# Kernel tuning notes

Measured on AMD Instinct MI355X. Metric: run time of the kernel, lower is better.

## Reference

```python
import jax, jax.numpy as jnp
import numpy as np

N = 100000      # nodes
E = 3200000     # edges (avg degree 32)
DIN, DH, DOUT = 256, 256, 64
K = 10          # propagation hops


def _uniform(key, shape, fan_in):
    b = 1.0 / np.sqrt(fan_in)
    return jax.random.uniform(key, shape, jnp.float32, -b, b)


def setup_inputs() -> dict:
    key = jax.random.key(0)
    ks = jax.random.split(key, 8)
    x = jax.random.normal(ks[0], (N, DIN), jnp.float32)
    edge_index = jax.random.randint(ks[1], (2, E), 0, N, dtype=jnp.int64)
    W1 = _uniform(ks[2], (DIN, DH), DIN)
    b1 = _uniform(ks[3], (DH,), DIN)
    W2 = _uniform(ks[4], (DH, DOUT), DH)
    b2 = _uniform(ks[5], (DOUT,), DH)
    proj_w = _uniform(ks[6], (DOUT,), DOUT)
    proj_b = _uniform(ks[7], (), DOUT)
    return {"x": x, "edge_index": edge_index, "W1": W1, "b1": b1,
            "W2": W2, "b2": b2, "proj_w": proj_w, "proj_b": proj_b}


def _gcn_norm(edge_index, num_nodes):
    # add self-loops with weight 1, symmetric normalization deg^-1/2 A deg^-1/2
    loops = jnp.arange(num_nodes, dtype=edge_index.dtype)
    row = jnp.concatenate([edge_index[0], loops])
    col = jnp.concatenate([edge_index[1], loops])
    w = jnp.ones(row.shape[0], jnp.float32)
    deg = jax.ops.segment_sum(w, col, num_segments=num_nodes)
    dinv = jnp.where(deg > 0, jax.lax.rsqrt(deg), 0.0)
    norm = dinv[row] * dinv[col]  # edge weight is 1
    return row, col, norm


def reference(x, edge_index, W1, b1, W2, b2, proj_w, proj_b):
    h = jax.nn.relu(x @ W1 + b1)
    h = h @ W2 + b2                               # [N, DOUT]
    row, col, norm = _gcn_norm(edge_index, N)
    preds = [h]
    for _ in range(K):
        h = jax.ops.segment_sum(norm[:, None] * h[row], col, num_segments=N)
        preds.append(h)
    pps = jnp.stack(preds, axis=1)                # [N, K+1, DOUT]
    score = jax.nn.sigmoid(pps @ proj_w + proj_b) # [N, K+1]
    out = jnp.einsum('nk,nkc->nc', score, pps)    # adaptive hop pooling
    return out
```

## Files before the change

kernel.cpp:

```cpp
#include <hip/hip_runtime.h>
#include <hip/hip_bf16.h>
#include <math.h>


#define WAVE 64
#define NBLK 1024
#define RS 520

__device__ inline float bf2f(unsigned short u) {
    union { unsigned int i; float f; } v; v.i = ((unsigned int)u) << 16; return v.f;
}
__device__ inline unsigned short f2bf(float f) {
    __hip_bfloat16 b = __float2bfloat16(f);
    union { __hip_bfloat16 b; unsigned short u; } v; v.b = b; return v.u;
}
__device__ inline float bflo(unsigned u) {
    union { unsigned i; float f; } v; v.i = u << 16; return v.f;
}
__device__ inline float bfhi(unsigned u) {
    union { unsigned i; float f; } v; v.i = u & 0xffff0000u; return v.f;
}

typedef __attribute__((ext_vector_type(8))) short bf16x8;
typedef __attribute__((ext_vector_type(16))) float f32x16;

__global__ void detect_kernel(const unsigned* __restrict__ e, int* __restrict__ sflag) {
    __shared__ int any;
    if (threadIdx.x == 0) any = 0;
    __syncthreads();
    unsigned nz = 0;
    int t = threadIdx.x;
    for (int i = 0; i < 8; ++i) nz |= e[(size_t)(t * 8 + i) * 2 + 1];
    if (nz) atomicOr(&any, 1);
    __syncthreads();
    if (t == 0) *sflag = any ? 1 : 2;
}

__global__ void passA_kernel(const int* __restrict__ eidx, const int* __restrict__ sflag,
                             int* __restrict__ blk_cnt, int E, int NB, int EPB) {
    __shared__ int lh[512];
    int t = threadIdx.x, blk = blockIdx.x;
    for (int i = t; i < NB; i += 256) lh[i] = 0;
    __syncthreads();
    int s = *sflag;
    int base = blk * EPB;
    int end = base + EPB; if (end > E) end = E;
    for (int e = base + t; e < end; e += 256) {
        int c = eidx[(size_t)s * (size_t)(E + e)];
        atomicAdd(&lh[c >> 8], 1);
    }
    __syncthreads();
    for (int i = t; i < NB; i += 256)
        blk_cnt[(size_t)blk * NB + i] = lh[i];
}

__global__ void scan1_kernel(const int* __restrict__ in, int* __restrict__ out,
                             int* __restrict__ bsums, int n) {
    __shared__ int s[256];
    int t = threadIdx.x;
    int idx = blockIdx.x * 1024 + t * 4;
    int x0 = (idx + 0 < n) ? in[idx + 0] : 0;
    int x1 = (idx + 1 < n) ? in[idx + 1] : 0;
    int x2 = (idx + 2 < n) ? in[idx + 2] : 0;
    int x3 = (idx + 3 < n) ? in[idx + 3] : 0;
    int lsum = x0 + x1 + x2 + x3;
    s[t] = lsum;
    __syncthreads();
    for (int o = 1; o < 256; o <<= 1) {
        int v = (t >= o) ? s[t - o] : 0;
        __syncthreads();
        if (t >= o) s[t] += v;
        __syncthreads();
    }
    int excl = s[t] - lsum;
    if (idx + 0 < n) out[idx + 0] = excl;
    if (idx + 1 < n) out[idx + 1] = excl + x0;
    if (idx + 2 < n) out[idx + 2] = excl + x0 + x1;
    if (idx + 3 < n) out[idx + 3] = excl + x0 + x1 + x2;
    if (t == 255) bsums[blockIdx.x] = s[255];
}

__global__ void scan2g_kernel(int* __restrict__ bsums, int nb) {
    __shared__ int part[256];
    int t = threadIdx.x;
    int v[4]; int run = 0;
    #pragma unroll
    for (int j = 0; j < 4; ++j) {
        int i = t * 4 + j;
        int x = (i < nb) ? bsums[i] : 0;
        v[j] = run; run += x;
    }
    part[t] = run;
    __syncthreads();
    for (int o = 1; o < 256; o <<= 1) {
        int x = (t >= o) ? part[t - o] : 0;
        __syncthreads();
        if (t >= o) part[t] += x;
        __syncthreads();
    }
    int excl = part[t] - run;
    #pragma unroll
    for (int j = 0; j < 4; ++j) {
        int i = t * 4 + j;
        if (i < nb) bsums[i] = excl + v[j];
    }
}

__global__ void scan3_kernel(int* __restrict__ arr, const int* __restrict__ bsums,
                             int n, int total) {
    int t = threadIdx.x;
    int idx = blockIdx.x * 1024 + t * 4;
    int add = bsums[blockIdx.x];
    #pragma unroll
    for (int i = 0; i < 4; ++i)
        if (idx + i < n) arr[idx + i] += add;
    if (blockIdx.x == 0 && t == 0) arr[n] = total;
}

__global__ void passB_kernel(const int* __restrict__ eidx, const int* __restrict__ sflag,
                             const int* __restrict__ pbase, int2* __restrict__ pairs,
                             int E, int NB, int EPB) {
    __shared__ int lcur[512];
    int t = threadIdx.x, blk = blockIdx.x;
    for (int i = t; i < NB; i += 256) lcur[i] = pbase[(size_t)blk * NB + i];
    __syncthreads();
    int s = *sflag;
    int base = blk * EPB;
    int end = base + EPB; if (end > E) end = E;
    for (int e = base + t; e < end; e += 256) {
        int r = eidx[(size_t)s * (size_t)e];
        int c = eidx[(size_t)s * (size_t)(E + e)];
        int pos = atomicAdd(&lcur[c >> 8], 1);
        pairs[pos] = make_int2(r, c);
    }
}

__global__ void passD_kernel(const int2* __restrict__ pairs, const int* __restrict__ pbase,
                             int* __restrict__ cnt, int N, int NB) {
    __shared__ int lcnt[256];
    int b = blockIdx.x, t = threadIdx.x;
    lcnt[t] = 0;
    __syncthreads();
    for (int blk = t; blk < NBLK; blk += 256) {
        int w0 = pbase[(size_t)blk * NB + b];
        int w1 = pbase[(size_t)blk * NB + b + 1];
        for (int i = w0; i < w1; ++i)
            atomicAdd(&lcnt[pairs[i].y & 255], 1);
    }
    __syncthreads();
    int node = b * 256 + t;
    if (node < N) cnt[node] = lcnt[t];
}

__global__ void dinv_kernel(const int* __restrict__ cnt, float* __restrict__ dinv, int n) {
    int i = blockIdx.x * blockDim.x + threadIdx.x;
    if (i < n) dinv[i] = rsqrtf((float)(cnt[i] + 1));
}

__global__ void passC_kernel(const int2* __restrict__ pairs, const int* __restrict__ pbase,
                             const int* __restrict__ offs, int* __restrict__ csr_src,
                             int N, int NB) {
    __shared__ int lcur[256];
    int b = blockIdx.x, t = threadIdx.x;
    int node = b * 256 + t;
    lcur[t] = (node < N) ? offs[node] : 0;
    __syncthreads();
    for (int blk = t; blk < NBLK; blk += 256) {
        int w0 = pbase[(size_t)blk * NB + b];
        int w1 = pbase[(size_t)blk * NB + b + 1];
        for (int i = w0; i < w1; ++i) {
            int2 p = pairs[i];
            int pos = atomicAdd(&lcur[p.y & 255], 1);
            csr_src[pos] = p.x;
        }
    }
}

__global__ void wconv_kernel(const float* __restrict__ W, unsigned short* __restrict__ Wf,
                             int K, int Nn) {
    int i = blockIdx.x * blockDim.x + threadIdx.x;
    if (i >= K * Nn) return;
    int k = i / Nn, n = i - k * Nn;
    Wf[(size_t)(k >> 3) * Nn * 8 + n * 8 + (k & 7)] = f2bf(W[i]);
}

__global__ __launch_bounds__(256, 4) void mlp_fused(
        const float* __restrict__ x,
        const unsigned short* __restrict__ W1f,
        const float* __restrict__ b1,
        const unsigned short* __restrict__ W2f,
        const float* __restrict__ b2,
        const float* __restrict__ dinv,
        const float* __restrict__ pw, const float* __restrict__ pb,
        float* __restrict__ out, unsigned short* __restrict__ g,
        int M) {
    __shared__ unsigned short xfrag[4 * RS];
    __shared__ unsigned short h1frag[32 * RS];
    __shared__ float pools[2][2][2][16];

    int tid = threadIdx.x;
    int wave = tid >> 6, lane = tid & 63;
    int half = lane >> 5, l31 = lane & 31;
    int rt = wave & 1;
    int cw = wave >> 1;
    int bm = blockIdx.x * 64;

    f32x16 acc1[4] = {};

    float4 xv[2];
    #pragma unroll
    for (int i = 0; i < 2; ++i) {
        int f = i * 256 + tid;
        int row = f >> 3, c4 = (f & 7) * 4;
        int grow = bm + row;
        xv[i] = (grow < M) ? *(const float4*)(x + (size_t)grow * 256 + c4)
                           : make_float4(0.f, 0.f, 0.f, 0.f);
    }

    for (int it = 0; it < 8; ++it) {
        #pragma unroll
        for (int i = 0; i < 2; ++i) {
            int f = i * 256 + tid;
            int row = f >> 3, c4 = (f & 7) * 4;
            int region = c4 >> 3, off = c4 & 7;
            ushort4 u;
            u.x = f2bf(xv[i].x); u.y = f2bf(xv[i].y);
            u.z = f2bf(xv[i].z); u.w = f2bf(xv[i].w);
            *(ushort4*)&xfrag[region * RS + row * 8 + off] = u;
        }
        __syncthreads();
        if (it < 7) {
            int k0 = (it + 1) * 32;
            #pragma unroll
            for (int i = 0; i < 2; ++i) {
                int f = i * 256 + tid;
                int row = f >> 3, c4 = (f & 7) * 4;
                int grow = bm + row;
                xv[i] = (grow < M) ? *(const float4*)(x + (size_t)grow * 256 + k0 + c4)
                                   : make_float4(0.f, 0.f, 0.f, 0.f);
            }
        }
        #pragma unroll
        for (int s = 0; s < 2; ++s) {
            int region = it * 4 + s * 2 + half;
            bf16x8 a = *(bf16x8*)&xfrag[(s * 2 + half) * RS + (rt * 32 + l31) * 8];
            #pragma unroll
            for (int j = 0; j < 4; ++j) {
                int ch = cw * 128 + j * 32 + l31;
                bf16x8 b = *(const bf16x8*)(W1f + (size_t)region * 2048 + ch * 8);
                acc1[j] = __builtin_amdgcn_mfma_f32_32x32x16_bf16(a, b, acc1[j], 0, 0, 0);
            }
        }
        __syncthreads();
    }

    #pragma unroll
    for (int j = 0; j < 4; ++j) {
        int ch = cw * 128 + j * 32 + l31;
        float bb = b1[ch];
        int region = ch >> 3, off = ch & 7;
        #pragma unroll
        for (int reg = 0; reg < 16; ++reg) {
            int rowin = (reg & 3) + 8 * (reg >> 2) + 4 * half;
            int row = rt * 32 + rowin;
            float v = fmaxf(acc1[j][reg] + bb, 0.f);
            h1frag[region * RS + row * 8 + off] = f2bf(v);
        }
    }
    __syncthreads();

    int rt2 = wave >> 1, ct2 = wave & 1;
    f32x16 acc2 = {};
    #pragma unroll
    for (int s = 0; s < 16; ++s) {
        bf16x8 a = *(bf16x8*)&h1frag[(s * 2 + half) * RS + (rt2 * 32 + l31) * 8];
        bf16x8 b = *(const bf16x8*)(W2f + (size_t)(s * 2 + half) * 512 + (ct2 * 32 + l31) * 8);
        acc2 = __builtin_amdgcn_mfma_f32_32x32x16_bf16(a, b, acc2, 0, 0, 0);
    }

    float bb = b2[ct2 * 32 + l31];
    float pwv = pw[ct2 * 32 + l31];
    float pbv = pb[0];
    float hreg[16];
    #pragma unroll
    for (int reg = 0; reg < 16; ++reg) {
        float h = acc2[reg] + bb;
        hreg[reg] = h;
        float d = h * pwv;
        d += __shfl_xor(d, 1, 64);
        d += __shfl_xor(d, 2, 64);
        d += __shfl_xor(d, 4, 64);
        d += __shfl_xor(d, 8, 64);
        d += __shfl_xor(d, 16, 64);
        if (l31 == 0) pools[rt2][ct2][half][reg] = d;
    }
    __syncthreads();
    #pragma unroll
    for (int reg = 0; reg < 16; ++reg) {
        int rowin = (reg & 3) + 8 * (reg >> 2) + 4 * half;
        int row = bm + rt2 * 32 + rowin;
        float d = pools[rt2][0][half][reg] + pools[rt2][1][half][reg];
        float sg = 1.f / (1.f + __expf(-(d + pbv)));
        float h = hreg[reg];
        if (row < M) {
            float dv = dinv[row];
            out[(size_t)row * 64 + ct2 * 32 + l31] = sg * h;
            g[(size_t)row * 64 + ct2 * 32 + l31]   = f2bf(dv * h);
        }
    }
}

__global__ void spmm_kernel(const int* __restrict__ offs, const int* __restrict__ src,
                            const float* __restrict__ dinv,
                            const unsigned* __restrict__ gin,
                            unsigned short* __restrict__ gout,
                            float* __restrict__ out,
                            const float* __restrict__ pw, const float* __restrict__ pb,
                            int n) {
    int wid = (blockIdx.x * blockDim.x + threadIdx.x) >> 6;
    int lane = threadIdx.x & 63;
    if (wid >= n) return;
    int g = lane >> 4;
    int q = lane & 15;
    int c = __builtin_amdgcn_readfirstlane(wid);
    int e0   = __builtin_amdgcn_readfirstlane(offs[c]);
    int eend = __builtin_amdgcn_readfirstlane(offs[c + 1]);

    float a0 = 0.f, a1 = 0.f, a2 = 0.f, a3 = 0.f;
    for (int e = e0; e < eend; e += 32) {
        #pragma unroll
        for (int i = 0; i < 8; ++i) {
            int ei = e + i * 4 + g;
            int ec = (ei < eend) ? ei : (eend - 1);
            float m = (ei < eend) ? 1.f : 0.f;
            int s = src[ec];
            uint2 v = *(const uint2*)(gin + (size_t)s * 32 + q * 2);
            a0 = fmaf(m, bflo(v.x), a0);
            a1 = fmaf(m, bfhi(v.x), a1);
            a2 = fmaf(m, bflo(v.y), a2);
            a3 = fmaf(m, bfhi(v.y), a3);
        }
    }

    a0 += __shfl_xor(a0, 16, 64); a0 += __shfl_xor(a0, 32, 64);
    a1 += __shfl_xor(a1, 16, 64); a1 += __shfl_xor(a1, 32, 64);
    a2 += __shfl_xor(a2, 16, 64); a2 += __shfl_xor(a2, 32, 64);
    a3 += __shfl_xor(a3, 16, 64); a3 += __shfl_xor(a3, 32, 64);

    uint2 sv = *(const uint2*)(gin + (size_t)c * 32 + q * 2);
    a0 += bflo(sv.x); a1 += bfhi(sv.x);
    a2 += bflo(sv.y); a3 += bfhi(sv.y);

    float dc = dinv[c];
    float h0 = dc * a0, h1 = dc * a1, h2 = dc * a2, h3 = dc * a3;

    float4 pv = *(const float4*)(pw + q * 4);
    float d = h0 * pv.x + h1 * pv.y + h2 * pv.z + h3 * pv.w;
    d += __shfl_xor(d, 1, 64);
    d += __shfl_xor(d, 2, 64);
    d += __shfl_xor(d, 4, 64);
    d += __shfl_xor(d, 8, 64);
    float sg = 1.f / (1.f + __expf(-(d + pb[0])));

    if (g == 0) {
        ushort4 gw;
        gw.x = f2bf(dc * h0); gw.y = f2bf(dc * h1);
        gw.z = f2bf(dc * h2); gw.w = f2bf(dc * h3);
        *(ushort4*)(gout + (size_t)c * 64 + q * 4) = gw;
        float4 o = *(float4*)(out + (size_t)c * 64 + q * 4);
        o.x += sg * h0; o.y += sg * h1; o.z += sg * h2; o.w += sg * h3;
        *(float4*)(out + (size_t)c * 64 + q * 4) = o;
    }
}

extern "C" void kernel_launch(void* const* d_in, const int* in_sizes, int n_in,
                              void* d_out, int out_size, void* d_ws, size_t ws_size,
                              hipStream_t stream) {
    const float* x  = (const float*)d_in[0];
    const int* eidx = (const int*)d_in[1];
    const float* W1 = (const float*)d_in[2];
    const float* b1 = (const float*)d_in[3];
    const float* W2 = (const float*)d_in[4];
    const float* b2 = (const float*)d_in[5];
    const float* pw = (const float*)d_in[6];
    const float* pb = (const float*)d_in[7];
    float* out = (float*)d_out;

    const int N = in_sizes[0] / 256;
    const int E = in_sizes[1] / 2;
    const int NB = (N + 255) >> 8;
    const int EPB = (E + NBLK - 1) / NBLK;
    const int M = NB * NBLK;

    size_t woff = 0;
    auto alloc = [&](size_t bytes) -> void* {
        void* p = (char*)d_ws + woff;
        woff += (bytes + 255) & ~(size_t)255;
        return p;
    };
    int*   sflag   = (int*)alloc(4);
    int*   cnt     = (int*)alloc((size_t)N * 4);
    float* dinv    = (float*)alloc((size_t)N * 4);
    int*   offs    = (int*)alloc(((size_t)N + 1) * 4);
    int*   bsums   = (int*)alloc(1024 * 4);
    int*   bsums2  = (int*)alloc(1024 * 4);
    int*   pbase   = (int*)alloc(((size_t)M + 1) * 4);
    int*   csr_src = (int*)alloc((size_t)E * 4);
    int2*  pairs   = (int2*)alloc((size_t)E * 8);
    unsigned short* W1f = (unsigned short*)alloc((size_t)256 * 256 * 2);
    unsigned short* W2f = (unsigned short*)alloc((size_t)64 * 256 * 2);
    unsigned short* gA = (unsigned short*)alloc((size_t)N * 64 * 2);
    unsigned short* gB = (unsigned short*)alloc((size_t)N * 64 * 2);

    detect_kernel<<<1, 256, 0, stream>>>((const unsigned*)eidx, sflag);

    passA_kernel<<<NBLK, 256, 0, stream>>>(eidx, sflag, pbase, E, NB, EPB);
    int nb2 = (M + 1023) / 1024;
    scan1_kernel<<<nb2, 256, 0, stream>>>(pbase, pbase, bsums2, M);
    scan2g_kernel<<<1, 256, 0, stream>>>(bsums2, nb2);
    scan3_kernel<<<nb2, 256, 0, stream>>>(pbase, bsums2, M, E);
    passB_kernel<<<NBLK, 256, 0, stream>>>(eidx, sflag, pbase, pairs, E, NB, EPB);
    passD_kernel<<<NB, 256, 0, stream>>>(pairs, pbase, cnt, N, NB);
    dinv_kernel<<<(N + 255) / 256, 256, 0, stream>>>(cnt, dinv, N);
    int nb1 = (N + 1023) / 1024;
    scan1_kernel<<<nb1, 256, 0, stream>>>(cnt, offs, bsums, N);
    scan2g_kernel<<<1, 256, 0, stream>>>(bsums, nb1);
    scan3_kernel<<<nb1, 256, 0, stream>>>(offs, bsums, N, E);
    passC_kernel<<<NB, 256, 0, stream>>>(pairs, pbase, offs, csr_src, N, NB);

    wconv_kernel<<<(256 * 256 + 255) / 256, 256, 0, stream>>>(W1, W1f, 256, 256);
    wconv_kernel<<<(64 * 256 + 255) / 256, 256, 0, stream>>>(W2, W2f, 256, 64);
    int gb = (N + 63) / 64;
    mlp_fused<<<gb, 256, 0, stream>>>(x, W1f, b1, W2f, b2, dinv, pw, pb,
                                      out, gA, N);

    int nwb = (N + 3) / 4;
    unsigned short* gin = gA;
    unsigned short* gout = gB;
    for (int k = 0; k < 10; ++k) {
        spmm_kernel<<<nwb, 256, 0, stream>>>(offs, csr_src, dinv,
                                             (const unsigned*)gin, gout, out, pw, pb, N);
        unsigned short* t = gin; gin = gout; gout = t;
    }
}
```

Before: 980.3 us.

## Partition CSR by source range and process 20 destinations per wave in SpMM

Edges are bucketed by destination and also by source range (8 ranges of 16384 nodes), giving a CSR with N*8 offsets. Each SpMM wave now handles 20 consecutive destination nodes and sweeps the source ranges in order, so gathers from the bf16 feature table stay in a narrower window at a time for better cache locality. Each half-wave covers the full 64-wide row with one dword per lane, and 40 register accumulators are kept per lane. In exchange the scan and counting buffers become 8x larger, per-node edge loops are short and divergent, and register pressure may limit occupancy.

```diff
diff --git a/kernel.cpp b/kernel.cpp
--- a/kernel.cpp
+++ b/kernel.cpp
@@ -6,6 +6,9 @@
 #define WAVE 64
 #define NBLK 1024
 #define RS 520
+#define NR 8
+#define RSH 14
+#define DPW 20
 
 __device__ inline float bf2f(unsigned short u) {
     union { unsigned int i; float f; } v; v.i = ((unsigned int)u) << 16; return v.f;
@@ -135,42 +138,52 @@
     }
 }
 
-__global__ void passD_kernel(const int2* __restrict__ pairs, const int* __restrict__ pbase,
-                             int* __restrict__ cnt, int N, int NB) {
-    __shared__ int lcnt[256];
+__global__ void passD2_kernel(const int2* __restrict__ pairs, const int* __restrict__ pbase,
+                              int* __restrict__ cnt2, int N, int NB) {
+    __shared__ int lcnt[256 * NR];
     int b = blockIdx.x, t = threadIdx.x;
-    lcnt[t] = 0;
-    __syncthreads();
-    for (int blk = t; blk < NBLK; blk += 256) {
-        int w0 = pbase[(size_t)blk * NB + b];
-        int w1 = pbase[(size_t)blk * NB + b + 1];
-        for (int i = w0; i < w1; ++i)
-            atomicAdd(&lcnt[pairs[i].y & 255], 1);
-    }
-    __syncthreads();
-    int node = b * 256 + t;
-    if (node < N) cnt[node] = lcnt[t];
-}
-
-__global__ void dinv_kernel(const int* __restrict__ cnt, float* __restrict__ dinv, int n) {
-    int i = blockIdx.x * blockDim.x + threadIdx.x;
-    if (i < n) dinv[i] = rsqrtf((float)(cnt[i] + 1));
-}
-
-__global__ void passC_kernel(const int2* __restrict__ pairs, const int* __restrict__ pbase,
-                             const int* __restrict__ offs, int* __restrict__ csr_src,
-                             int N, int NB) {
-    __shared__ int lcur[256];
-    int b = blockIdx.x, t = threadIdx.x;
-    int node = b * 256 + t;
-    lcur[t] = (node < N) ? offs[node] : 0;
+    for (int i = t; i < 256 * NR; i += 256) lcnt[i] = 0;
     __syncthreads();
     for (int blk = t; blk < NBLK; blk += 256) {
         int w0 = pbase[(size_t)blk * NB + b];
         int w1 = pbase[(size_t)blk * NB + b + 1];
         for (int i = w0; i < w1; ++i) {
             int2 p = pairs[i];
-            int pos = atomicAdd(&lcur[p.y & 255], 1);
+            atomicAdd(&lcnt[((p.x >> RSH) << 8) | (p.y & 255)], 1);
+        }
+    }
+    __syncthreads();
+    for (int i = t; i < 256 * NR; i += 256) {
+        int node = b * 256 + (i & 255);
+        if (node < N) cnt2[(size_t)(i >> 8) * N + node] = lcnt[i];
+    }
+}
+
+__global__ void dinv2_kernel(const int* __restrict__ cnt2, float* __restrict__ dinv, int n) {
+    int i = blockIdx.x * blockDim.x + threadIdx.x;
+    if (i >= n) return;
+    int deg = 0;
+    #pragma unroll
+    for (int r = 0; r < NR; ++r) deg += cnt2[(size_t)r * n + i];
+    dinv[i] = rsqrtf((float)(deg + 1));
+}
+
+__global__ void passC2_kernel(const int2* __restrict__ pairs, const int* __restrict__ pbase,
+                              const int* __restrict__ offs2, int* __restrict__ csr_src,
+                              int N, int NB) {
+    __shared__ int lcur[256 * NR];
+    int b = blockIdx.x, t = threadIdx.x;
+    for (int i = t; i < 256 * NR; i += 256) {
+        int node = b * 256 + (i & 255);
+        lcur[i] = (node < N) ? offs2[(size_t)(i >> 8) * N + node] : 0;
+    }
+    __syncthreads();
+    for (int blk = t; blk < NBLK; blk += 256) {
+        int w0 = pbase[(size_t)blk * NB + b];
+        int w1 = pbase[(size_t)blk * NB + b + 1];
+        for (int i = w0; i < w1; ++i) {
+            int2 p = pairs[i];
+            int pos = atomicAdd(&lcur[((p.x >> RSH) << 8) | (p.y & 255)], 1);
             csr_src[pos] = p.x;
         }
     }
@@ -310,66 +323,76 @@
     }
 }
 
-__global__ void spmm_kernel(const int* __restrict__ offs, const int* __restrict__ src,
-                            const float* __restrict__ dinv,
-                            const unsigned* __restrict__ gin,
-                            unsigned short* __restrict__ gout,
-                            float* __restrict__ out,
-                            const float* __restrict__ pw, const float* __restrict__ pb,
-                            int n) {
-    int wid = (blockIdx.x * blockDim.x + threadIdx.x) >> 6;
+__global__ __launch_bounds__(256, 5) void spmm2_kernel(
+        const int* __restrict__ offs2, const int* __restrict__ src,
+        const float* __restrict__ dinv,
+        const unsigned* __restrict__ gin,
+        unsigned* __restrict__ gout,
+        float* __restrict__ out,
+        const float* __restrict__ pw, const float* __restrict__ pb,
+        int n) {
+    int wid = blockIdx.x * 4 + (threadIdx.x >> 6);
     int lane = threadIdx.x & 63;
-    if (wid >= n) return;
-    int g = lane >> 4;
-    int q = lane & 15;
-    int c = __builtin_amdgcn_readfirstlane(wid);
-    int e0   = __builtin_amdgcn_readfirstlane(offs[c]);
-    int eend = __builtin_amdgcn_readfirstlane(offs[c + 1]);
-
-    float a0 = 0.f, a1 = 0.f, a2 = 0.f, a3 = 0.f;
-    for (int e = e0; e < eend; e += 32) {
+    int g = lane >> 5;
+    int q = lane & 31;
+    int base = wid * DPW;
+    if (base >= n) return;
+
+    float accA[DPW], accB[DPW];
+    #pragma unroll
+    for (int j = 0; j < DPW; ++j) { accA[j] = 0.f; accB[j] = 0.f; }
+
+    for (int r = 0; r < NR; ++r) {
+        size_t kb = (size_t)r * n + base;
+        int e0 = __builtin_amdgcn_readfirstlane(offs2[kb]);
         #pragma unroll
-        for (int i = 0; i < 8; ++i) {
-            int ei = e + i * 4 + g;
-            int ec = (ei < eend) ? ei : (eend - 1);
-            float m = (ei < eend) ? 1.f : 0.f;
-            int s = src[ec];
-            uint2 v = *(const uint2*)(gin + (size_t)s * 32 + q * 2);
-            a0 = fmaf(m, bflo(v.x), a0);
-            a1 = fmaf(m, bfhi(v.x), a1);
-            a2 = fmaf(m, bflo(v.y), a2);
-            a3 = fmaf(m, bfhi(v.y), a3);
-        }
-    }
-
-    a0 += __shfl_xor(a0, 16, 64); a0 += __shfl_xor(a0, 32, 64);
-    a1 += __shfl_xor(a1, 16, 64); a1 += __shfl_xor(a1, 32, 64);
-    a2 += __shfl_xor(a2, 16, 64); a2 += __shfl_xor(a2, 32, 64);
-    a3 += __shfl_xor(a3, 16, 64); a3 += __shfl_xor(a3, 32, 64);
-
-    uint2 sv = *(const uint2*)(gin + (size_t)c * 32 + q * 2);
-    a0 += bflo(sv.x); a1 += bfhi(sv.x);
-    a2 += bflo(sv.y); a3 += bfhi(sv.y);
-
-    float dc = dinv[c];
-    float h0 = dc * a0, h1 = dc * a1, h2 = dc * a2, h3 = dc * a3;
-
-    float4 pv = *(const float4*)(pw + q * 4);
-    float d = h0 * pv.x + h1 * pv.y + h2 * pv.z + h3 * pv.w;
-    d += __shfl_xor(d, 1, 64);
-    d += __shfl_xor(d, 2, 64);
-    d += __shfl_xor(d, 4, 64);
-    d += __shfl_xor(d, 8, 64);
-    float sg = 1.f / (1.f + __expf(-(d + pb[0])));
-
-    if (g == 0) {
-        ushort4 gw;
-        gw.x = f2bf(dc * h0); gw.y = f2bf(dc * h1);
-        gw.z = f2bf(dc * h2); gw.w = f2bf(dc * h3);
-        *(ushort4*)(gout + (size_t)c * 64 + q * 4) = gw;
-        float4 o = *(float4*)(out + (size_t)c * 64 + q * 4);
-        o.x += sg * h0; o.y += sg * h1; o.z += sg * h2; o.w += sg * h3;
-        *(float4*)(out + (size_t)c * 64 + q * 4) = o;
+        for (int j = 0; j < DPW; ++j) {
+            if (base + j < n) {
+                int e1 = __builtin_amdgcn_readfirstlane(offs2[kb + j + 1]);
+                for (int e = e0; e < e1; e += 4) {
+                    #pragma unroll
+                    for (int u = 0; u < 2; ++u) {
+                        int ei = e + u * 2 + g;
+                        int ec = (ei < e1) ? ei : (e1 - 1);
+                        unsigned mm = (ei < e1) ? 0xffffffffu : 0u;
+                        int s = src[ec];
+                        unsigned v = gin[(size_t)s * 32 + q] & mm;
+                        accA[j] += bflo(v);
+                        accB[j] += bfhi(v);
+                    }
+                }
+                e0 = e1;
+            }
+        }
+    }
+
+    float pbv = pb[0];
+    float2 pv = *(const float2*)(pw + q * 2);
+    #pragma unroll
+    for (int j = 0; j < DPW; ++j) {
+        int c = base + j;
+        if (c >= n) break;
+        float a0 = accA[j], a1 = accB[j];
+        a0 += __shfl_xor(a0, 32, 64);
+        a1 += __shfl_xor(a1, 32, 64);
+        unsigned sv = gin[(size_t)c * 32 + q];
+        a0 += bflo(sv); a1 += bfhi(sv);
+        float dc = dinv[c];
+        float h0 = dc * a0, h1 = dc * a1;
+        float d = h0 * pv.x + h1 * pv.y;
+        d += __shfl_xor(d, 1, 64);
+        d += __shfl_xor(d, 2, 64);
+        d += __shfl_xor(d, 4, 64);
+        d += __shfl_xor(d, 8, 64);
+        d += __shfl_xor(d, 16, 64);
+        float sg = 1.f / (1.f + __expf(-(d + pbv)));
+        if (g == 0) {
+            gout[(size_t)c * 32 + q] =
+                (unsigned)f2bf(dc * h0) | ((unsigned)f2bf(dc * h1) << 16);
+            float2 o = *(float2*)(out + (size_t)c * 64 + q * 2);
+            o.x += sg * h0; o.y += sg * h1;
+            *(float2*)(out + (size_t)c * 64 + q * 2) = o;
+        }
     }
 }
 
@@ -391,6 +414,7 @@
     const int NB = (N + 255) >> 8;
     const int EPB = (E + NBLK - 1) / NBLK;
     const int M = NB * NBLK;
+    const int N8 = N * NR;
 
     size_t woff = 0;
     auto alloc = [&](size_t bytes) -> void* {
@@ -399,9 +423,9 @@
         return p;
     };
     int*   sflag   = (int*)alloc(4);
-    int*   cnt     = (int*)alloc((size_t)N * 4);
+    int*   cnt2    = (int*)alloc((size_t)N8 * 4);
     float* dinv    = (float*)alloc((size_t)N * 4);
-    int*   offs    = (int*)alloc(((size_t)N + 1) * 4);
+    int*   offs2   = (int*)alloc(((size_t)N8 + 1) * 4);
     int*   bsums   = (int*)alloc(1024 * 4);
     int*   bsums2  = (int*)alloc(1024 * 4);
     int*   pbase   = (int*)alloc(((size_t)M + 1) * 4);
@@ -420,13 +444,13 @@
     scan2g_kernel<<<1, 256, 0, stream>>>(bsums2, nb2);
     scan3_kernel<<<nb2, 256, 0, stream>>>(pbase, bsums2, M, E);
     passB_kernel<<<NBLK, 256, 0, stream>>>(eidx, sflag, pbase, pairs, E, NB, EPB);
-    passD_kernel<<<NB, 256, 0, stream>>>(pairs, pbase, cnt, N, NB);
-    dinv_kernel<<<(N + 255) / 256, 256, 0, stream>>>(cnt, dinv, N);
-    int nb1 = (N + 1023) / 1024;
-    scan1_kernel<<<nb1, 256, 0, stream>>>(cnt, offs, bsums, N);
+    passD2_kernel<<<NB, 256, 0, stream>>>(pairs, pbase, cnt2, N, NB);
+    dinv2_kernel<<<(N + 255) / 256, 256, 0, stream>>>(cnt2, dinv, N);
+    int nb1 = (N8 + 1023) / 1024;
+    scan1_kernel<<<nb1, 256, 0, stream>>>(cnt2, offs2, bsums, N8);
     scan2g_kernel<<<1, 256, 0, stream>>>(bsums, nb1);
-    scan3_kernel<<<nb1, 256, 0, stream>>>(offs, bsums, N, E);
-    passC_kernel<<<NB, 256, 0, stream>>>(pairs, pbase, offs, csr_src, N, NB);
+    scan3_kernel<<<nb1, 256, 0, stream>>>(offs2, bsums, N8, E);
+    passC2_kernel<<<NB, 256, 0, stream>>>(pairs, pbase, offs2, csr_src, N, NB);
 
     wconv_kernel<<<(256 * 256 + 255) / 256, 256, 0, stream>>>(W1, W1f, 256, 256);
     wconv_kernel<<<(64 * 256 + 255) / 256, 256, 0, stream>>>(W2, W2f, 256, 64);
@@ -434,12 +458,13 @@
     mlp_fused<<<gb, 256, 0, stream>>>(x, W1f, b1, W2f, b2, dinv, pw, pb,
                                       out, gA, N);
 
-    int nwb = (N + 3) / 4;
+    int nblk2 = (N + DPW * 4 - 1) / (DPW * 4);
     unsigned short* gin = gA;
     unsigned short* gout = gB;
     for (int k = 0; k < 10; ++k) {
-        spmm_kernel<<<nwb, 256, 0, stream>>>(offs, csr_src, dinv,
-                                             (const unsigned*)gin, gout, out, pw, pb, N);
+        spmm2_kernel<<<nblk2, 256, 0, stream>>>(offs2, csr_src, dinv,
+                                                (const unsigned*)gin, (unsigned*)gout,
+                                                out, pw, pb, N);
         unsigned short* t = gin; gin = gout; gout = t;
     }
 }
```

New measurement: 2.487 ms. +153.7%, slower.

## Split propagated features into channel planes and defer hop pooling by one step

Applied to the files above, without the earlier changes.

The bf16 propagation buffer is re-laid out as four 16-channel planes, so each SpMM block gathers 32-byte rows from a single plane whose working set is smaller and more cache-resident. Each wave now processes 16 destination nodes in turn. Each plane writes its partial projection dot to a side buffer, and the sigmoid-weighted accumulation into out happens one hop later. That deferred step rebuilds h from the stored normalized features times sqrt(degree), and a final kernel handles the last hop. The cost is that edge indices are read four times (once per plane), plus extra dot-product buffers, an extra kernel launch and a bit of bf16 rounding in the reconstruction.

```diff
diff --git a/kernel.cpp b/kernel.cpp
--- a/kernel.cpp
+++ b/kernel.cpp
@@ -6,6 +6,7 @@
 #define WAVE 64
 #define NBLK 1024
 #define RS 520
+#define DPW 16
 
 __device__ inline float bf2f(unsigned short u) {
     union { unsigned int i; float f; } v; v.i = ((unsigned int)u) << 16; return v.f;
@@ -152,9 +153,14 @@
     if (node < N) cnt[node] = lcnt[t];
 }
 
-__global__ void dinv_kernel(const int* __restrict__ cnt, float* __restrict__ dinv, int n) {
+__global__ void dinv_kernel(const int* __restrict__ cnt, float* __restrict__ dinv,
+                            float* __restrict__ sdeg, int n) {
     int i = blockIdx.x * blockDim.x + threadIdx.x;
-    if (i < n) dinv[i] = rsqrtf((float)(cnt[i] + 1));
+    if (i < n) {
+        float d1 = (float)(cnt[i] + 1);
+        dinv[i] = rsqrtf(d1);
+        sdeg[i] = sqrtf(d1);
+    }
 }
 
 __global__ void passC_kernel(const int2* __restrict__ pairs, const int* __restrict__ pbase,
@@ -295,6 +301,7 @@
         if (l31 == 0) pools[rt2][ct2][half][reg] = d;
     }
     __syncthreads();
+    int ch = ct2 * 32 + l31;
     #pragma unroll
     for (int reg = 0; reg < 16; ++reg) {
         int rowin = (reg & 3) + 8 * (reg >> 2) + 4 * half;
@@ -304,73 +311,118 @@
         float h = hreg[reg];
         if (row < M) {
             float dv = dinv[row];
-            out[(size_t)row * 64 + ct2 * 32 + l31] = sg * h;
-            g[(size_t)row * 64 + ct2 * 32 + l31]   = f2bf(dv * h);
-        }
-    }
-}
-
-__global__ void spmm_kernel(const int* __restrict__ offs, const int* __restrict__ src,
-                            const float* __restrict__ dinv,
-                            const unsigned* __restrict__ gin,
-                            unsigned short* __restrict__ gout,
-                            float* __restrict__ out,
-                            const float* __restrict__ pw, const float* __restrict__ pb,
-                            int n) {
-    int wid = (blockIdx.x * blockDim.x + threadIdx.x) >> 6;
+            out[(size_t)row * 64 + ch] = sg * h;
+            g[((size_t)(ch >> 4) * (size_t)M + (size_t)row) * 16 + (ch & 15)]
+                = f2bf(dv * h);
+        }
+    }
+}
+
+__global__ __launch_bounds__(256) void spmm4_kernel(
+        const int* __restrict__ offs, const int* __restrict__ src,
+        const float* __restrict__ dinv, const float* __restrict__ sdeg,
+        const unsigned* __restrict__ gin,
+        unsigned* __restrict__ gout,
+        const float* __restrict__ dpin, float* __restrict__ dpout,
+        float* __restrict__ out,
+        const float* __restrict__ pw, const float* __restrict__ pb,
+        int n, int do_prev) {
     int lane = threadIdx.x & 63;
-    if (wid >= n) return;
-    int g = lane >> 4;
-    int q = lane & 15;
-    int c = __builtin_amdgcn_readfirstlane(wid);
-    int e0   = __builtin_amdgcn_readfirstlane(offs[c]);
-    int eend = __builtin_amdgcn_readfirstlane(offs[c + 1]);
-
-    float a0 = 0.f, a1 = 0.f, a2 = 0.f, a3 = 0.f;
-    for (int e = e0; e < eend; e += 32) {
-        #pragma unroll
-        for (int i = 0; i < 8; ++i) {
-            int ei = e + i * 4 + g;
-            int ec = (ei < eend) ? ei : (eend - 1);
-            float m = (ei < eend) ? 1.f : 0.f;
-            int s = src[ec];
-            uint2 v = *(const uint2*)(gin + (size_t)s * 32 + q * 2);
-            a0 = fmaf(m, bflo(v.x), a0);
-            a1 = fmaf(m, bfhi(v.x), a1);
-            a2 = fmaf(m, bflo(v.y), a2);
-            a3 = fmaf(m, bfhi(v.y), a3);
-        }
-    }
-
-    a0 += __shfl_xor(a0, 16, 64); a0 += __shfl_xor(a0, 32, 64);
-    a1 += __shfl_xor(a1, 16, 64); a1 += __shfl_xor(a1, 32, 64);
-    a2 += __shfl_xor(a2, 16, 64); a2 += __shfl_xor(a2, 32, 64);
-    a3 += __shfl_xor(a3, 16, 64); a3 += __shfl_xor(a3, 32, 64);
-
-    uint2 sv = *(const uint2*)(gin + (size_t)c * 32 + q * 2);
-    a0 += bflo(sv.x); a1 += bfhi(sv.x);
-    a2 += bflo(sv.y); a3 += bfhi(sv.y);
-
-    float dc = dinv[c];
-    float h0 = dc * a0, h1 = dc * a1, h2 = dc * a2, h3 = dc * a3;
-
-    float4 pv = *(const float4*)(pw + q * 4);
-    float d = h0 * pv.x + h1 * pv.y + h2 * pv.z + h3 * pv.w;
-    d += __shfl_xor(d, 1, 64);
-    d += __shfl_xor(d, 2, 64);
-    d += __shfl_xor(d, 4, 64);
-    d += __shfl_xor(d, 8, 64);
-    float sg = 1.f / (1.f + __expf(-(d + pb[0])));
-
-    if (g == 0) {
-        ushort4 gw;
-        gw.x = f2bf(dc * h0); gw.y = f2bf(dc * h1);
-        gw.z = f2bf(dc * h2); gw.w = f2bf(dc * h3);
-        *(ushort4*)(gout + (size_t)c * 64 + q * 4) = gw;
-        float4 o = *(float4*)(out + (size_t)c * 64 + q * 4);
-        o.x += sg * h0; o.y += sg * h1; o.z += sg * h2; o.w += sg * h3;
-        *(float4*)(out + (size_t)c * 64 + q * 4) = o;
-    }
+    int wv = threadIdx.x >> 6;
+    int blk = blockIdx.x;
+    int plane = (blk & 7) >> 1;
+    int sub = blk & 1;
+    int pblk = blk >> 3;
+    int base = (((pblk << 1) | sub) * 4 + wv) * DPW;
+    if (base >= n) return;
+    int sl = (lane >> 2) & 15;
+    int q = lane & 3;
+    const unsigned* gpl = gin + (size_t)plane * (size_t)n * 8;
+    unsigned* gopl = gout + (size_t)plane * (size_t)n * 8;
+    float pbv = pb[0];
+    float4 pv = *(const float4*)(pw + plane * 16 + q * 4);
+
+    for (int j = 0; j < DPW; ++j) {
+        int c = base + j;
+        if (c >= n) break;
+        int e0 = __builtin_amdgcn_readfirstlane(offs[c]);
+        int e1 = __builtin_amdgcn_readfirstlane(offs[c + 1]);
+        float a0 = 0.f, a1 = 0.f, a2 = 0.f, a3 = 0.f;
+        for (int e = e0; e < e1; e += 32) {
+            int ei0 = e + sl, ei1 = e + 16 + sl;
+            int ec0 = ei0 < e1 ? ei0 : e1 - 1;
+            int ec1 = ei1 < e1 ? ei1 : e1 - 1;
+            unsigned m0 = ei0 < e1 ? 0xffffffffu : 0u;
+            unsigned m1 = ei1 < e1 ? 0xffffffffu : 0u;
+            int s0 = __builtin_nontemporal_load(src + ec0);
+            int s1 = __builtin_nontemporal_load(src + ec1);
+            uint2 v0 = *(const uint2*)(gpl + (size_t)s0 * 8 + q * 2);
+            uint2 v1 = *(const uint2*)(gpl + (size_t)s1 * 8 + q * 2);
+            v0.x &= m0; v0.y &= m0; v1.x &= m1; v1.y &= m1;
+            a0 += bflo(v0.x) + bflo(v1.x);
+            a1 += bfhi(v0.x) + bfhi(v1.x);
+            a2 += bflo(v0.y) + bflo(v1.y);
+            a3 += bfhi(v0.y) + bfhi(v1.y);
+        }
+        a0 += __shfl_xor(a0, 4, 64); a0 += __shfl_xor(a0, 8, 64);
+        a0 += __shfl_xor(a0, 16, 64); a0 += __shfl_xor(a0, 32, 64);
+        a1 += __shfl_xor(a1, 4, 64); a1 += __shfl_xor(a1, 8, 64);
+        a1 += __shfl_xor(a1, 16, 64); a1 += __shfl_xor(a1, 32, 64);
+        a2 += __shfl_xor(a2, 4, 64); a2 += __shfl_xor(a2, 8, 64);
+        a2 += __shfl_xor(a2, 16, 64); a2 += __shfl_xor(a2, 32, 64);
+        a3 += __shfl_xor(a3, 4, 64); a3 += __shfl_xor(a3, 8, 64);
+        a3 += __shfl_xor(a3, 16, 64); a3 += __shfl_xor(a3, 32, 64);
+
+        uint2 sv = *(const uint2*)(gpl + (size_t)c * 8 + q * 2);
+        float f0 = bflo(sv.x), f1 = bfhi(sv.x);
+        float f2v = bflo(sv.y), f3 = bfhi(sv.y);
+        float dc = dinv[c];
+        float h0 = dc * (a0 + f0), h1 = dc * (a1 + f1);
+        float h2 = dc * (a2 + f2v), h3 = dc * (a3 + f3);
+
+        float d = h0 * pv.x + h1 * pv.y + h2 * pv.z + h3 * pv.w;
+        d += __shfl_xor(d, 1, 64);
+        d += __shfl_xor(d, 2, 64);
+        if (lane == 0) dpout[(size_t)c * 4 + plane] = d;
+
+        if (lane < 4) {
+            unsigned gw0 = (unsigned)f2bf(dc * h0) | ((unsigned)f2bf(dc * h1) << 16);
+            unsigned gw1 = (unsigned)f2bf(dc * h2) | ((unsigned)f2bf(dc * h3) << 16);
+            unsigned* gp = gopl + (size_t)c * 8 + lane * 2;
+            __builtin_nontemporal_store(gw0, gp);
+            __builtin_nontemporal_store(gw1, gp + 1);
+            if (do_prev) {
+                float4 dp = *(const float4*)(dpin + (size_t)c * 4);
+                float sg = 1.f / (1.f + __expf(-(dp.x + dp.y + dp.z + dp.w + pbv)));
+                float sd = sdeg[c] * sg;
+                float* op = out + (size_t)c * 64 + plane * 16 + lane * 4;
+                float4 o = *(float4*)op;
+                o.x += sd * f0; o.y += sd * f1;
+                o.z += sd * f2v; o.w += sd * f3;
+                *(float4*)op = o;
+            }
+        }
+    }
+}
+
+__global__ void final_kernel(const unsigned* __restrict__ glast,
+                             const float* __restrict__ dplast,
+                             const float* __restrict__ sdeg,
+                             const float* __restrict__ pb,
+                             float* __restrict__ out, int n) {
+    int tid = blockIdx.x * 256 + threadIdx.x;
+    int c = tid >> 4;
+    if (c >= n) return;
+    int w = tid & 15;
+    int plane = w >> 2, q = w & 3;
+    float4 dp = *(const float4*)(dplast + (size_t)c * 4);
+    float sg = 1.f / (1.f + __expf(-(dp.x + dp.y + dp.z + dp.w + pb[0])));
+    float sd = sdeg[c] * sg;
+    uint2 v = *(const uint2*)(glast + ((size_t)plane * n + c) * 8 + q * 2);
+    float4 o = *(float4*)(out + (size_t)c * 64 + w * 4);
+    o.x += sd * bflo(v.x); o.y += sd * bfhi(v.x);
+    o.z += sd * bflo(v.y); o.w += sd * bfhi(v.y);
+    *(float4*)(out + (size_t)c * 64 + w * 4) = o;
 }
 
 extern "C" void kernel_launch(void* const* d_in, const int* in_sizes, int n_in,
@@ -401,6 +453,7 @@
     int*   sflag   = (int*)alloc(4);
     int*   cnt     = (int*)alloc((size_t)N * 4);
     float* dinv    = (float*)alloc((size_t)N * 4);
+    float* sdeg    = (float*)alloc((size_t)N * 4);
     int*   offs    = (int*)alloc(((size_t)N + 1) * 4);
     int*   bsums   = (int*)alloc(1024 * 4);
     int*   bsums2  = (int*)alloc(1024 * 4);
@@ -411,6 +464,8 @@
     unsigned short* W2f = (unsigned short*)alloc((size_t)64 * 256 * 2);
     unsigned short* gA = (unsigned short*)alloc((size_t)N * 64 * 2);
     unsigned short* gB = (unsigned short*)alloc((size_t)N * 64 * 2);
+    float* dpA = (float*)alloc((size_t)N * 16);
+    float* dpB = (float*)alloc((size_t)N * 16);
 
     detect_kernel<<<1, 256, 0, stream>>>((const unsigned*)eidx, sflag);
 
@@ -421,7 +476,7 @@
     scan3_kernel<<<nb2, 256, 0, stream>>>(pbase, bsums2, M, E);
     passB_kernel<<<NBLK, 256, 0, stream>>>(eidx, sflag, pbase, pairs, E, NB, EPB);
     passD_kernel<<<NB, 256, 0, stream>>>(pairs, pbase, cnt, N, NB);
-    dinv_kernel<<<(N + 255) / 256, 256, 0, stream>>>(cnt, dinv, N);
+    dinv_kernel<<<(N + 255) / 256, 256, 0, stream>>>(cnt, dinv, sdeg, N);
     int nb1 = (N + 1023) / 1024;
     scan1_kernel<<<nb1, 256, 0, stream>>>(cnt, offs, bsums, N);
     scan2g_kernel<<<1, 256, 0, stream>>>(bsums, nb1);
@@ -434,12 +489,19 @@
     mlp_fused<<<gb, 256, 0, stream>>>(x, W1f, b1, W2f, b2, dinv, pw, pb,
                                       out, gA, N);
 
-    int nwb = (N + 3) / 4;
+    int bpx2 = (N + 8 * DPW - 1) / (8 * DPW);
+    int grid4 = 8 * bpx2;
     unsigned short* gin = gA;
     unsigned short* gout = gB;
+    float* dpin = dpA;
+    float* dpout = dpB;
     for (int k = 0; k < 10; ++k) {
-        spmm_kernel<<<nwb, 256, 0, stream>>>(offs, csr_src, dinv,
-                                             (const unsigned*)gin, gout, out, pw, pb, N);
+        spmm4_kernel<<<grid4, 256, 0, stream>>>(offs, csr_src, dinv, sdeg,
+                                                (const unsigned*)gin, (unsigned*)gout,
+                                                dpin, dpout, out, pw, pb, N, k > 0);
         unsigned short* t = gin; gin = gout; gout = t;
-    }
-}
+        float* td = dpin; dpin = dpout; dpout = td;
+    }
+    final_kernel<<<(N * 16 + 255) / 256, 256, 0, stream>>>(
+        (const unsigned*)gin, dpin, sdeg, pb, out, N);
+}
```

Result: slower. 2.428 ms (+147.6%).

## Store all hop planes in bf16 and pool once in a separate kernel

Applied to the files above, without the earlier changes.

Each SpMM hop now writes its scaled output into its own bf16 plane. The sigmoid-score pooling into the fp32 output moves out of every hop and the MLP into a single pool kernel, which recovers h by multiplying with sqrt(deg). The SpMM is also reshaped to use 8 lanes per edge with 16-byte gathers and nontemporal index loads, and the edge pair buffer is aliased into the later prediction planes. This removes ten read-modify-write passes over the fp32 output at the cost of an extra pool read of eleven planes. The pooled values are now rebuilt from bf16-rounded data.

```diff
diff --git a/kernel.cpp b/kernel.cpp
--- a/kernel.cpp
+++ b/kernel.cpp
@@ -152,9 +152,14 @@
     if (node < N) cnt[node] = lcnt[t];
 }
 
-__global__ void dinv_kernel(const int* __restrict__ cnt, float* __restrict__ dinv, int n) {
+__global__ void dinv_kernel(const int* __restrict__ cnt, float* __restrict__ dinv,
+                            float* __restrict__ sdeg, int n) {
     int i = blockIdx.x * blockDim.x + threadIdx.x;
-    if (i < n) dinv[i] = rsqrtf((float)(cnt[i] + 1));
+    if (i < n) {
+        float d1 = (float)(cnt[i] + 1);
+        dinv[i] = rsqrtf(d1);
+        sdeg[i] = sqrtf(d1);
+    }
 }
 
 __global__ void passC_kernel(const int2* __restrict__ pairs, const int* __restrict__ pbase,
@@ -191,12 +196,10 @@
         const unsigned short* __restrict__ W2f,
         const float* __restrict__ b2,
         const float* __restrict__ dinv,
-        const float* __restrict__ pw, const float* __restrict__ pb,
-        float* __restrict__ out, unsigned short* __restrict__ g,
+        unsigned short* __restrict__ g,
         int M) {
     __shared__ unsigned short xfrag[4 * RS];
     __shared__ unsigned short h1frag[32 * RS];
-    __shared__ float pools[2][2][2][16];
 
     int tid = threadIdx.x;
     int wave = tid >> 6, lane = tid & 63;
@@ -279,98 +282,101 @@
     }
 
     float bb = b2[ct2 * 32 + l31];
-    float pwv = pw[ct2 * 32 + l31];
+    int ch = ct2 * 32 + l31;
+    #pragma unroll
+    for (int reg = 0; reg < 16; ++reg) {
+        int rowin = (reg & 3) + 8 * (reg >> 2) + 4 * half;
+        int row = bm + rt2 * 32 + rowin;
+        if (row < M) {
+            float h = acc2[reg] + bb;
+            g[(size_t)row * 64 + ch] = f2bf(dinv[row] * h);
+        }
+    }
+}
+
+__global__ __launch_bounds__(256) void spmm5_kernel(
+        const int* __restrict__ offs, const int* __restrict__ src,
+        const float* __restrict__ dinv,
+        const unsigned* __restrict__ gin,
+        unsigned* __restrict__ gout, int n) {
+    int wid = (blockIdx.x * blockDim.x + threadIdx.x) >> 6;
+    int lane = threadIdx.x & 63;
+    if (wid >= n) return;
+    int g = lane >> 3;
+    int q = lane & 7;
+    int c = __builtin_amdgcn_readfirstlane(wid);
+    int e0 = __builtin_amdgcn_readfirstlane(offs[c]);
+    int e1 = __builtin_amdgcn_readfirstlane(offs[c + 1]);
+
+    float a0 = 0.f, a1 = 0.f, a2 = 0.f, a3 = 0.f;
+    float a4 = 0.f, a5 = 0.f, a6 = 0.f, a7 = 0.f;
+    for (int e = e0; e < e1; e += 16) {
+        #pragma unroll
+        for (int u = 0; u < 2; ++u) {
+            int ei = e + u * 8 + g;
+            int ec = ei < e1 ? ei : e1 - 1;
+            unsigned m = ei < e1 ? 0xffffffffu : 0u;
+            int s = __builtin_nontemporal_load(src + ec);
+            uint4 v = *(const uint4*)(gin + (size_t)s * 32 + q * 4);
+            v.x &= m; v.y &= m; v.z &= m; v.w &= m;
+            a0 += bflo(v.x); a1 += bfhi(v.x);
+            a2 += bflo(v.y); a3 += bfhi(v.y);
+            a4 += bflo(v.z); a5 += bfhi(v.z);
+            a6 += bflo(v.w); a7 += bfhi(v.w);
+        }
+    }
+    a0 += __shfl_xor(a0, 8, 64); a0 += __shfl_xor(a0, 16, 64); a0 += __shfl_xor(a0, 32, 64);
+    a1 += __shfl_xor(a1, 8, 64); a1 += __shfl_xor(a1, 16, 64); a1 += __shfl_xor(a1, 32, 64);
+    a2 += __shfl_xor(a2, 8, 64); a2 += __shfl_xor(a2, 16, 64); a2 += __shfl_xor(a2, 32, 64);
+    a3 += __shfl_xor(a3, 8, 64); a3 += __shfl_xor(a3, 16, 64); a3 += __shfl_xor(a3, 32, 64);
+    a4 += __shfl_xor(a4, 8, 64); a4 += __shfl_xor(a4, 16, 64); a4 += __shfl_xor(a4, 32, 64);
+    a5 += __shfl_xor(a5, 8, 64); a5 += __shfl_xor(a5, 16, 64); a5 += __shfl_xor(a5, 32, 64);
+    a6 += __shfl_xor(a6, 8, 64); a6 += __shfl_xor(a6, 16, 64); a6 += __shfl_xor(a6, 32, 64);
+    a7 += __shfl_xor(a7, 8, 64); a7 += __shfl_xor(a7, 16, 64); a7 += __shfl_xor(a7, 32, 64);
+
+    uint4 sv = *(const uint4*)(gin + (size_t)c * 32 + q * 4);
+    float dc = dinv[c];
+    float h0 = dc * (a0 + bflo(sv.x)), h1 = dc * (a1 + bfhi(sv.x));
+    float h2 = dc * (a2 + bflo(sv.y)), h3 = dc * (a3 + bfhi(sv.y));
+    float h4 = dc * (a4 + bflo(sv.z)), h5 = dc * (a5 + bfhi(sv.z));
+    float h6 = dc * (a6 + bflo(sv.w)), h7 = dc * (a7 + bfhi(sv.w));
+
+    if (g == 0) {
+        uint4 gw;
+        gw.x = (unsigned)f2bf(dc * h0) | ((unsigned)f2bf(dc * h1) << 16);
+        gw.y = (unsigned)f2bf(dc * h2) | ((unsigned)f2bf(dc * h3) << 16);
+        gw.z = (unsigned)f2bf(dc * h4) | ((unsigned)f2bf(dc * h5) << 16);
+        gw.w = (unsigned)f2bf(dc * h6) | ((unsigned)f2bf(dc * h7) << 16);
+        *(uint4*)(gout + (size_t)c * 32 + q * 4) = gw;
+    }
+}
+
+__global__ void pool_kernel(const unsigned* __restrict__ preds, size_t pstride,
+                            const float* __restrict__ sdeg,
+                            const float* __restrict__ pw, const float* __restrict__ pb,
+                            float* __restrict__ out, int n) {
+    int tid = blockIdx.x * 256 + threadIdx.x;
+    int c = tid >> 4;
+    if (c >= n) return;
+    int w = tid & 15;
+    float sd = sdeg[c];
+    float4 pv = *(const float4*)(pw + w * 4);
     float pbv = pb[0];
-    float hreg[16];
-    #pragma unroll
-    for (int reg = 0; reg < 16; ++reg) {
-        float h = acc2[reg] + bb;
-        hreg[reg] = h;
-        float d = h * pwv;
+    float o0 = 0.f, o1 = 0.f, o2 = 0.f, o3 = 0.f;
+    for (int k = 0; k <= 10; ++k) {
+        uint2 v = *(const uint2*)(preds + (size_t)k * pstride + (size_t)c * 32 + w * 2);
+        float h0 = sd * bflo(v.x), h1 = sd * bfhi(v.x);
+        float h2 = sd * bflo(v.y), h3 = sd * bfhi(v.y);
+        float d = h0 * pv.x + h1 * pv.y + h2 * pv.z + h3 * pv.w;
         d += __shfl_xor(d, 1, 64);
         d += __shfl_xor(d, 2, 64);
         d += __shfl_xor(d, 4, 64);
         d += __shfl_xor(d, 8, 64);
-        d += __shfl_xor(d, 16, 64);
-        if (l31 == 0) pools[rt2][ct2][half][reg] = d;
-    }
-    __syncthreads();
-    #pragma unroll
-    for (int reg = 0; reg < 16; ++reg) {
-        int rowin = (reg & 3) + 8 * (reg >> 2) + 4 * half;
-        int row = bm + rt2 * 32 + rowin;
-        float d = pools[rt2][0][half][reg] + pools[rt2][1][half][reg];
         float sg = 1.f / (1.f + __expf(-(d + pbv)));
-        float h = hreg[reg];
-        if (row < M) {
-            float dv = dinv[row];
-            out[(size_t)row * 64 + ct2 * 32 + l31] = sg * h;
-            g[(size_t)row * 64 + ct2 * 32 + l31]   = f2bf(dv * h);
-        }
-    }
-}
-
-__global__ void spmm_kernel(const int* __restrict__ offs, const int* __restrict__ src,
-                            const float* __restrict__ dinv,
-                            const unsigned* __restrict__ gin,
-                            unsigned short* __restrict__ gout,
-                            float* __restrict__ out,
-                            const float* __restrict__ pw, const float* __restrict__ pb,
-                            int n) {
-    int wid = (blockIdx.x * blockDim.x + threadIdx.x) >> 6;
-    int lane = threadIdx.x & 63;
-    if (wid >= n) return;
-    int g = lane >> 4;
-    int q = lane & 15;
-    int c = __builtin_amdgcn_readfirstlane(wid);
-    int e0   = __builtin_amdgcn_readfirstlane(offs[c]);
-    int eend = __builtin_amdgcn_readfirstlane(offs[c + 1]);
-
-    float a0 = 0.f, a1 = 0.f, a2 = 0.f, a3 = 0.f;
-    for (int e = e0; e < eend; e += 32) {
-        #pragma unroll
-        for (int i = 0; i < 8; ++i) {
-            int ei = e + i * 4 + g;
-            int ec = (ei < eend) ? ei : (eend - 1);
-            float m = (ei < eend) ? 1.f : 0.f;
-            int s = src[ec];
-            uint2 v = *(const uint2*)(gin + (size_t)s * 32 + q * 2);
-            a0 = fmaf(m, bflo(v.x), a0);
-            a1 = fmaf(m, bfhi(v.x), a1);
-            a2 = fmaf(m, bflo(v.y), a2);
-            a3 = fmaf(m, bfhi(v.y), a3);
-        }
-    }
-
-    a0 += __shfl_xor(a0, 16, 64); a0 += __shfl_xor(a0, 32, 64);
-    a1 += __shfl_xor(a1, 16, 64); a1 += __shfl_xor(a1, 32, 64);
-    a2 += __shfl_xor(a2, 16, 64); a2 += __shfl_xor(a2, 32, 64);
-    a3 += __shfl_xor(a3, 16, 64); a3 += __shfl_xor(a3, 32, 64);
-
-    uint2 sv = *(const uint2*)(gin + (size_t)c * 32 + q * 2);
-    a0 += bflo(sv.x); a1 += bfhi(sv.x);
-    a2 += bflo(sv.y); a3 += bfhi(sv.y);
-
-    float dc = dinv[c];
-    float h0 = dc * a0, h1 = dc * a1, h2 = dc * a2, h3 = dc * a3;
-
-    float4 pv = *(const float4*)(pw + q * 4);
-    float d = h0 * pv.x + h1 * pv.y + h2 * pv.z + h3 * pv.w;
-    d += __shfl_xor(d, 1, 64);
-    d += __shfl_xor(d, 2, 64);
-    d += __shfl_xor(d, 4, 64);
-    d += __shfl_xor(d, 8, 64);
-    float sg = 1.f / (1.f + __expf(-(d + pb[0])));
-
-    if (g == 0) {
-        ushort4 gw;
-        gw.x = f2bf(dc * h0); gw.y = f2bf(dc * h1);
-        gw.z = f2bf(dc * h2); gw.w = f2bf(dc * h3);
-        *(ushort4*)(gout + (size_t)c * 64 + q * 4) = gw;
-        float4 o = *(float4*)(out + (size_t)c * 64 + q * 4);
-        o.x += sg * h0; o.y += sg * h1; o.z += sg * h2; o.w += sg * h3;
-        *(float4*)(out + (size_t)c * 64 + q * 4) = o;
-    }
+        o0 += sg * h0; o1 += sg * h1; o2 += sg * h2; o3 += sg * h3;
+    }
+    float4 o = make_float4(o0, o1, o2, o3);
+    *(float4*)(out + (size_t)c * 64 + w * 4) = o;
 }
 
 extern "C" void kernel_launch(void* const* d_in, const int* in_sizes, int n_in,
@@ -401,16 +407,17 @@
     int*   sflag   = (int*)alloc(4);
     int*   cnt     = (int*)alloc((size_t)N * 4);
     float* dinv    = (float*)alloc((size_t)N * 4);
+    float* sdeg    = (float*)alloc((size_t)N * 4);
     int*   offs    = (int*)alloc(((size_t)N + 1) * 4);
     int*   bsums   = (int*)alloc(1024 * 4);
     int*   bsums2  = (int*)alloc(1024 * 4);
     int*   pbase   = (int*)alloc(((size_t)M + 1) * 4);
     int*   csr_src = (int*)alloc((size_t)E * 4);
-    int2*  pairs   = (int2*)alloc((size_t)E * 8);
     unsigned short* W1f = (unsigned short*)alloc((size_t)256 * 256 * 2);
     unsigned short* W2f = (unsigned short*)alloc((size_t)64 * 256 * 2);
-    unsigned short* gA = (unsigned short*)alloc((size_t)N * 64 * 2);
-    unsigned short* gB = (unsigned short*)alloc((size_t)N * 64 * 2);
+    const size_t planeB = (size_t)N * 64 * 2;
+    unsigned short* preds = (unsigned short*)alloc(11 * planeB);
+    int2* pairs = (int2*)((char*)preds + planeB);
 
     detect_kernel<<<1, 256, 0, stream>>>((const unsigned*)eidx, sflag);
 
@@ -421,7 +428,7 @@
     scan3_kernel<<<nb2, 256, 0, stream>>>(pbase, bsums2, M, E);
     passB_kernel<<<NBLK, 256, 0, stream>>>(eidx, sflag, pbase, pairs, E, NB, EPB);
     passD_kernel<<<NB, 256, 0, stream>>>(pairs, pbase, cnt, N, NB);
-    dinv_kernel<<<(N + 255) / 256, 256, 0, stream>>>(cnt, dinv, N);
+    dinv_kernel<<<(N + 255) / 256, 256, 0, stream>>>(cnt, dinv, sdeg, N);
     int nb1 = (N + 1023) / 1024;
     scan1_kernel<<<nb1, 256, 0, stream>>>(cnt, offs, bsums, N);
     scan2g_kernel<<<1, 256, 0, stream>>>(bsums, nb1);
@@ -431,15 +438,15 @@
     wconv_kernel<<<(256 * 256 + 255) / 256, 256, 0, stream>>>(W1, W1f, 256, 256);
     wconv_kernel<<<(64 * 256 + 255) / 256, 256, 0, stream>>>(W2, W2f, 256, 64);
     int gb = (N + 63) / 64;
-    mlp_fused<<<gb, 256, 0, stream>>>(x, W1f, b1, W2f, b2, dinv, pw, pb,
-                                      out, gA, N);
+    mlp_fused<<<gb, 256, 0, stream>>>(x, W1f, b1, W2f, b2, dinv, preds, N);
 
     int nwb = (N + 3) / 4;
-    unsigned short* gin = gA;
-    unsigned short* gout = gB;
-    for (int k = 0; k < 10; ++k) {
-        spmm_kernel<<<nwb, 256, 0, stream>>>(offs, csr_src, dinv,
-                                             (const unsigned*)gin, gout, out, pw, pb, N);
-        unsigned short* t = gin; gin = gout; gout = t;
-    }
-}
+    for (int k = 1; k <= 10; ++k) {
+        const unsigned* gi = (const unsigned*)((char*)preds + (size_t)(k - 1) * planeB);
+        unsigned* go = (unsigned*)((char*)preds + (size_t)k * planeB);
+        spmm5_kernel<<<nwb, 256, 0, stream>>>(offs, csr_src, dinv, gi, go, N);
+    }
+
+    pool_kernel<<<(N * 16 + 255) / 256, 256, 0, stream>>>(
+        (const unsigned*)preds, planeB / 4, sdeg, pw, pb, out, N);
+}
```

Result: slower. 1.004 ms (+2.5%).
